# Kernel optimization log

Hardware: AMD Instinct MI355X
Metric: run time of the kernel (lower is better)

The kernel has to match this reference:

```python
import jax, jax.numpy as jnp
import numpy as np

B, N, D = 2, 2048, 1024
H, DH = 16, 64
EPS = 1e-5


def _layernorm(t, g, b):
    m = jnp.mean(t, axis=-1, keepdims=True)
    v = jnp.mean(jnp.square(t - m), axis=-1, keepdims=True)
    return (t - m) * jax.lax.rsqrt(v + EPS) * g + b


def setup_inputs() -> dict:
    key = jax.random.key(0)
    ks = jax.random.split(key, 4)
    return {
        "x": jax.random.normal(ks[0], (B, N, D), dtype=jnp.float32),
        "ln_g": jnp.ones((D,), jnp.float32),
        "ln_b": jnp.zeros((D,), jnp.float32),
        "lnc_g": jnp.ones((D,), jnp.float32),
        "lnc_b": jnp.zeros((D,), jnp.float32),
        "Wq": jax.random.normal(ks[1], (D, H * DH), jnp.float32) * 0.02,
        "Wkv": jax.random.normal(ks[2], (D, 2 * H * DH), jnp.float32) * 0.02,
        "Wo": jax.random.normal(ks[3], (H * DH, D), jnp.float32) * 0.02,
    }


def reference(x, ln_g, ln_b, lnc_g, lnc_b, Wq, Wkv, Wo):
    scale = DH ** (-0.5)
    xn = _layernorm(x, ln_g, ln_b)          # self-attn: context = x
    cn = _layernorm(x, lnc_g, lnc_b)
    q = xn @ Wq                              # [b, n, h*d]
    kv = cn @ Wkv
    k, v = jnp.split(kv, 2, axis=-1)
    # b n (h d) -> b h n d
    q = q.reshape(B, N, H, DH).transpose(0, 2, 1, 3)
    k = k.reshape(B, N, H, DH).transpose(0, 2, 1, 3)
    v = v.reshape(B, N, H, DH).transpose(0, 2, 1, 3)
    sim = jnp.einsum("bhnd,bhmd->bhnm", q, k) * scale
    neg = -jnp.finfo(sim.dtype).max
    causal = jnp.tril(jnp.ones((N, N), dtype=bool))  # allow j <= i
    sim = jnp.where(causal[None, None], sim, neg)
    attn = jax.nn.softmax(sim.astype(jnp.float32), axis=-1)
    out = jnp.einsum("bhnm,bhmd->bhnd", attn, v)
    out = out.transpose(0, 2, 1, 3).reshape(B, N, H * DH)
    return out @ Wo
```

## Files before the change

kernel.cpp:

```cpp
#include <hip/hip_runtime.h>
#include <hip/hip_bf16.h>

#define B_  2
#define N_  2048
#define D_  1024
#define H_  16
#define DH_ 64
#define BN_ROWS (B_ * N_)
#define EPS_ 1e-5f
#define QKV_N 3072

typedef __attribute__((ext_vector_type(8))) short bf16x8_t;
typedef __attribute__((ext_vector_type(4))) short bf16x4_t;
typedef __attribute__((ext_vector_type(4))) float f32x4_t;

#define MFMA16(a, b, c) __builtin_amdgcn_mfma_f32_16x16x16bf16_1k(a, b, c, 0, 0, 0)

typedef const unsigned int __attribute__((address_space(1)))* gas_ptr;
typedef unsigned int __attribute__((address_space(3)))* las_ptr;

__device__ __forceinline__ void async16(const unsigned short* g, unsigned short* l) {
    __builtin_amdgcn_global_load_lds((gas_ptr)g, (las_ptr)l, 16, 0, 0);
}

__device__ __forceinline__ unsigned short f2bf(float f) {
    unsigned int u = __float_as_uint(f);
    unsigned int r = u + 0x7FFFu + ((u >> 16) & 1u);
    return (unsigned short)(r >> 16);
}

__device__ __forceinline__ unsigned int pk2bf(float a, float b) {
    __hip_bfloat162 t = __float22bfloat162_rn(float2{a, b});
    return *(unsigned int*)&t;
}

__global__ __launch_bounds__(256) void ln_wt_kernel(
    const float* __restrict__ x,
    const float* __restrict__ g1, const float* __restrict__ b1,
    const float* __restrict__ g2, const float* __restrict__ b2,
    const float* __restrict__ Wq, const float* __restrict__ Wkv,
    const float* __restrict__ Wo,
    unsigned short* __restrict__ xn, unsigned short* __restrict__ cn,
    unsigned short* __restrict__ wqkvT, unsigned short* __restrict__ woT) {
    const int bid = blockIdx.x;
    const int tid = threadIdx.x;

    if (bid < BN_ROWS) {
        const int row = bid;
        const float4 v = ((const float4*)(x + (size_t)row * D_))[tid];

        float s  = v.x + v.y + v.z + v.w;
        float s2 = v.x * v.x + v.y * v.y + v.z * v.z + v.w * v.w;
        #pragma unroll
        for (int off = 32; off > 0; off >>= 1) {
            s  += __shfl_down(s,  off);
            s2 += __shfl_down(s2, off);
        }
        __shared__ float red[8];
        if ((tid & 63) == 0) { red[tid >> 6] = s; red[4 + (tid >> 6)] = s2; }
        __syncthreads();
        const float S  = red[0] + red[1] + red[2] + red[3];
        const float S2 = red[4] + red[5] + red[6] + red[7];
        const float mean = S * (1.0f / D_);
        const float var  = S2 * (1.0f / D_) - mean * mean;
        const float rstd = rsqrtf(var + EPS_);

        const float4 G1 = ((const float4*)g1)[tid];
        const float4 B1 = ((const float4*)b1)[tid];
        const float4 G2 = ((const float4*)g2)[tid];
        const float4 B2 = ((const float4*)b2)[tid];

        float nx[4] = { (v.x - mean) * rstd, (v.y - mean) * rstd,
                        (v.z - mean) * rstd, (v.w - mean) * rstd };
        ushort4 o1, o2;
        o1.x = f2bf(nx[0] * G1.x + B1.x); o1.y = f2bf(nx[1] * G1.y + B1.y);
        o1.z = f2bf(nx[2] * G1.z + B1.z); o1.w = f2bf(nx[3] * G1.w + B1.w);
        o2.x = f2bf(nx[0] * G2.x + B2.x); o2.y = f2bf(nx[1] * G2.y + B2.y);
        o2.z = f2bf(nx[2] * G2.z + B2.z); o2.w = f2bf(nx[3] * G2.w + B2.w);
        ((ushort4*)(xn + (size_t)row * D_))[tid] = o1;
        ((ushort4*)(cn + (size_t)row * D_))[tid] = o2;
    } else {
        const int zz = bid - BN_ROWS;
        const float* src;
        unsigned short* dst;
        int N, t;
        if (zz < 1024)      { src = Wq;  dst = wqkvT;                       N = 1024; t = zz; }
        else if (zz < 3072) { src = Wkv; dst = wqkvT + (size_t)1024 * 1024; N = 2048; t = zz - 1024; }
        else                { src = Wo;  dst = woT;                         N = 1024; t = zz - 3072; }
        const int nb = N / 32;
        const int n0 = (t % nb) * 32, k0 = (t / nb) * 32;

        __shared__ float tile[32][33];
        const int tx = tid & 31, ty = tid >> 5;
        #pragma unroll
        for (int i = 0; i < 4; i++)
            tile[ty + i * 8][tx] = src[(size_t)(k0 + ty + i * 8) * N + n0 + tx];
        __syncthreads();
        #pragma unroll
        for (int i = 0; i < 4; i++)
            dst[(size_t)(n0 + ty + i * 8) * 1024 + k0 + tx] = f2bf(tile[tx][ty + i * 8]);
    }
}

template <int BM, bool FUSED, bool BF16OUT, int MINW>
__global__ __launch_bounds__(256, MINW) void gemm_kernel(
    const unsigned short* __restrict__ A0, const unsigned short* __restrict__ A1,
    const unsigned short* __restrict__ Bt, void* __restrict__ Cv,
    unsigned short* __restrict__ vt, int M, int N, int K) {
    constexpr int WM = BM / 2, MT = WM / 16, AI = BM / 32;
    __shared__ unsigned short As[BM * 64];
    __shared__ unsigned short Bs[128 * 64];
    const int tid = threadIdx.x, lane = tid & 63, w = tid >> 6;
    const int quad = lane >> 4, l16 = lane & 15;
    const int lr8 = lane >> 3, pg8 = lane & 7;
    const int wr = (w >> 1) * WM, wc = (w & 1) * 64;
    const int bm = blockIdx.y * BM, bn = blockIdx.x * 128;
    const unsigned short* A = (FUSED && bn >= 1024) ? A1 : A0;
    const float cscale = (FUSED && bn < 1024) ? 0.180336880111120f : 1.0f;

    f32x4_t acc[MT][4] = {};
    for (int k0 = 0; k0 < K; k0 += 64) {
        #pragma unroll
        for (int i = 0; i < AI; i++) {
            const int rb = w * (BM / 4) + i * 8;
            const int r  = rb + lr8;
            const int g  = pg8 ^ (r & 7);
            async16(&A[(size_t)(bm + r) * K + k0 + g * 8], &As[rb * 64]);
        }
        #pragma unroll
        for (int i = 0; i < 4; i++) {
            const int rb = w * 32 + i * 8;
            const int r  = rb + lr8;
            const int g  = pg8 ^ (r & 7);
            async16(&Bt[(size_t)(bn + r) * K + k0 + g * 8], &Bs[rb * 64]);
        }
        __syncthreads();
        #pragma unroll
        for (int kk = 0; kk < 64; kk += 32) {
            bf16x8_t af[MT], bfr[4];
            const int g0 = (kk >> 3) + quad;
            #pragma unroll
            for (int t = 0; t < MT; t++)
                af[t] = *(const bf16x8_t*)&As[(wr + t * 16 + l16) * 64 +
                                              ((g0 ^ (l16 & 7)) * 8)];
            #pragma unroll
            for (int t = 0; t < 4; t++)
                bfr[t] = *(const bf16x8_t*)&Bs[(wc + t * 16 + l16) * 64 +
                                               ((g0 ^ (l16 & 7)) * 8)];
            #pragma unroll
            for (int mt = 0; mt < MT; mt++)
                #pragma unroll
                for (int nt = 0; nt < 4; nt++)
                    acc[mt][nt] = __builtin_amdgcn_mfma_f32_16x16x32_bf16(
                        af[mt], bfr[nt], acc[mt][nt], 0, 0, 0);
        }
        __syncthreads();
    }

    if (FUSED && bn >= 2048) {
        const int seq0 = bm + wr;
        const int bq = seq0 >> 11;
        const int kt = (seq0 & (N_ - 1)) >> 6;
        #pragma unroll
        for (int nt = 0; nt < 4; nt++) {
            const int c = (bn - 2048) + wc + nt * 16 + l16;
            unsigned short* dst =
                vt + (((size_t)(bq * 32 + kt) * 1024) + c) * 64;
            #pragma unroll
            for (int mt = 0; mt < 4; mt++) {
                uint2 v2 = { pk2bf(acc[mt][nt][0], acc[mt][nt][1]),
                             pk2bf(acc[mt][nt][2], acc[mt][nt][3]) };
                *(uint2*)&dst[mt * 16 + quad * 4] = v2;
            }
        }
        return;
    }

    #pragma unroll
    for (int mt = 0; mt < MT; mt++)
        #pragma unroll
        for (int nt = 0; nt < 4; nt++)
            #pragma unroll
            for (int r = 0; r < 4; r++) {
                const int row = bm + wr + mt * 16 + quad * 4 + r;
                const int col = bn + wc + nt * 16 + l16;
                if (BF16OUT)
                    ((unsigned short*)Cv)[(size_t)row * N + col] =
                        f2bf(acc[mt][nt][r] * cscale);
                else
                    ((float*)Cv)[(size_t)row * N + col] = acc[mt][nt][r];
            }
}

__global__ __launch_bounds__(256, 2) void flash_attn_kernel(
    const unsigned short* __restrict__ qkv, const unsigned short* __restrict__ vt,
    unsigned short* __restrict__ out) {
    __shared__ unsigned short Qs[64 * 64];
    __shared__ unsigned short Ks[2][64 * 64];
    __shared__ unsigned short Vts[3][64 * 64];

    const int tid = threadIdx.x, lane = tid & 63, w = tid >> 6;
    const int quad = lane >> 4, l16 = lane & 15;
    const int lr8 = lane >> 3, pg8 = lane & 7;
    const int bid = blockIdx.x;
    const int bh   = (bid & 7) * 4 + ((bid >> 3) & 3);
    const int pair = bid >> 5;
    const int b = bh >> 4, h = bh & 15;

    const unsigned short* qb  = qkv + (size_t)(b * N_) * QKV_N + h * DH_;
    const unsigned short* kb  = qb + 1024;
    const unsigned short* vtb = vt + ((size_t)(b * 32) * 1024 + h * 64) * 64;

    bf16x4_t ones4;
    #pragma unroll
    for (int j = 0; j < 4; j++) ones4[j] = (short)0x3F80;

    for (int phase = 0; phase < 2; phase++) {
        const int qt = phase ? (31 - pair) : pair;
        const int qs = qt * 64;
        const int niter = qt + 1;

        __syncthreads();

        f32x4_t o[4] = {};
        f32x4_t lacc = {};
        bf16x8_t qf[2];
        bf16x4_t pf[4];

        auto prefetch = [&](int t) {
            const int ksel = t & 1, vsel = t % 3;
            #pragma unroll
            for (int i = 0; i < 2; i++) {
                const int rb = w * 16 + i * 8;
                const int r  = rb + lr8;
                const int g  = pg8 ^ (r & 7);
                async16(&kb[(size_t)(t * 64 + r) * QKV_N + g * 8],
                        &Ks[ksel][rb * 64]);
                async16(&vtb[((size_t)t * 1024 + r) * 64 + g * 8],
                        &Vts[vsel][rb * 64]);
            }
        };
        auto do_qk = [&](int kbuf, f32x4_t* s) {
            __builtin_amdgcn_s_setprio(1);
            #pragma unroll
            for (int k2 = 0; k2 < 2; k2++) {
                const int g0 = k2 * 4 + quad;
                #pragma unroll
                for (int kt = 0; kt < 4; kt++) {
                    const bf16x8_t a = *(const bf16x8_t*)&Ks[kbuf][
                        (kt * 16 + l16) * 64 + (g0 ^ (l16 & 7)) * 8];
                    s[kt] = __builtin_amdgcn_mfma_f32_16x16x32_bf16(
                        a, qf[k2], s[kt], 0, 0, 0);
                }
            }
            __builtin_amdgcn_s_setprio(0);
        };
        auto do_exp = [&](const f32x4_t* s, int js, bool edge) {
            #pragma unroll
            for (int kt = 0; kt < 4; kt++) {
                float p[4];
                #pragma unroll
                for (int r = 0; r < 4; r++) {
                    float sv = s[kt][r];
                    if (edge) {
                        const int key = js + kt * 16 + quad * 4 + r;
                        const int qy  = qs + w * 16 + l16;
                        if (key > qy) sv = -3e38f;
                    }
                    p[r] = __builtin_amdgcn_exp2f(sv);
                }
                uint2 pk = { pk2bf(p[0], p[1]), pk2bf(p[2], p[3]) };
                pf[kt] = *(bf16x4_t*)&pk;
            }
        };
        auto do_pv = [&](int vbuf) {
            __builtin_amdgcn_s_setprio(1);
            #pragma unroll
            for (int kt = 0; kt < 4; kt++) {
                const int g = kt * 2 + (quad >> 1);
                const int col = ((g ^ (l16 & 7)) * 8) + (quad & 1) * 4;
                #pragma unroll
                for (int nt = 0; nt < 4; nt++) {
                    const bf16x4_t bv = *(const bf16x4_t*)&Vts[vbuf][
                        (nt * 16 + l16) * 64 + col];
                    o[nt] = MFMA16(pf[kt], bv, o[nt]);
                }
                lacc = MFMA16(pf[kt], ones4, lacc);
            }
            __builtin_amdgcn_s_setprio(0);
        };

        #pragma unroll
        for (int i = 0; i < 2; i++) {
            const int rb = w * 16 + i * 8;
            const int r  = rb + lr8;
            const int g  = pg8 ^ (r & 7);
            async16(&qb[(size_t)(qs + r) * QKV_N + g * 8], &Qs[rb * 64]);
        }
        prefetch(0);
        __syncthreads();

        if (niter > 1) prefetch(1);
        #pragma unroll
        for (int k2 = 0; k2 < 2; k2++) {
            const int g0 = k2 * 4 + quad;
            qf[k2] = *(const bf16x8_t*)&Qs[
                (w * 16 + l16) * 64 + (g0 ^ (l16 & 7)) * 8];
        }
        {
            f32x4_t s[4] = {};
            do_qk(0, s);
            do_exp(s, 0, niter == 1);
        }

        for (int jt = 1; jt < niter; jt++) {
            __syncthreads();
            if (jt + 1 < niter) prefetch(jt + 1);
            f32x4_t s[4] = {};
            do_qk(jt & 1, s);
            do_pv((jt - 1) % 3);
            do_exp(s, jt * 64, jt == niter - 1);
        }
        do_pv((niter - 1) % 3);

        #pragma unroll
        for (int r = 0; r < 4; r++) {
            const float inv = 1.0f / lacc[r];
            const int query = qs + w * 16 + quad * 4 + r;
            const int row = b * N_ + query;
            #pragma unroll
            for (int nt = 0; nt < 4; nt++) {
                const int col = h * DH_ + nt * 16 + l16;
                out[(size_t)row * (H_ * DH_) + col] = f2bf(o[nt][r] * inv);
            }
        }
    }
}

extern "C" void kernel_launch(void* const* d_in, const int* in_sizes, int n_in,
                              void* d_out, int out_size, void* d_ws, size_t ws_size,
                              hipStream_t stream) {
    const float* x     = (const float*)d_in[0];
    const float* ln_g  = (const float*)d_in[1];
    const float* ln_b  = (const float*)d_in[2];
    const float* lnc_g = (const float*)d_in[3];
    const float* lnc_b = (const float*)d_in[4];
    const float* Wq    = (const float*)d_in[5];
    const float* Wkv   = (const float*)d_in[6];
    const float* Wo    = (const float*)d_in[7];

    char* ws = (char*)d_ws;
    const size_t MB = 1024 * 1024;
    unsigned short* qkv   = (unsigned short*)(ws + 0 * MB);
    unsigned short* vtbuf = (unsigned short*)(ws + 24 * MB);
    unsigned short* xn    = (unsigned short*)(ws + 32 * MB);
    unsigned short* cn    = (unsigned short*)(ws + 40 * MB);
    unsigned short* wqkvT = (unsigned short*)(ws + 48 * MB);
    unsigned short* woT   = (unsigned short*)(ws + 54 * MB);
    unsigned short* ao    = xn;

    ln_wt_kernel<<<8192, 256, 0, stream>>>(
        x, ln_g, ln_b, lnc_g, lnc_b, Wq, Wkv, Wo, xn, cn, wqkvT, woT);

    gemm_kernel<128, true, true, 3>
        <<<dim3(QKV_N / 128, BN_ROWS / 128), 256, 0, stream>>>(
        xn, cn, wqkvT, qkv, vtbuf, BN_ROWS, QKV_N, D_);

    flash_attn_kernel<<<B_ * H_ * 16, 256, 0, stream>>>(qkv, vtbuf, ao);

    gemm_kernel<64, false, false, 2>
        <<<dim3(D_ / 128, BN_ROWS / 64), 256, 0, stream>>>(
        ao, nullptr, woT, (float*)d_out, nullptr, BN_ROWS, D_, H_ * DH_);
}
```

Measured before the change: 182.5 us.

## Split attention key tile across two wave groups with LDS reduction

Doubles the flash-attention block to 512 threads (8 waves), where each group of four waves handles half of each 64-key tile for the same 16 query rows. At the end, the partial output and row sums from the second group are written to shared memory and added by the first group before normalization and store. The goal is more waves per CU to hide latency and halve per-wave MFMA work per tile, at the cost of an extra LDS reduction, two extra barriers, and the removal of s_setprio hints. No max-subtraction is used, so the partial sums can be added directly.

```diff
diff --git a/kernel.cpp b/kernel.cpp
--- a/kernel.cpp
+++ b/kernel.cpp
@@ -192,7 +192,7 @@
             }
 }
 
-__global__ __launch_bounds__(256, 2) void flash_attn_kernel(
+__global__ __launch_bounds__(512, 4) void flash_attn_kernel(
     const unsigned short* __restrict__ qkv, const unsigned short* __restrict__ vt,
     unsigned short* __restrict__ out) {
     __shared__ unsigned short Qs[64 * 64];
@@ -202,6 +202,8 @@
     const int tid = threadIdx.x, lane = tid & 63, w = tid >> 6;
     const int quad = lane >> 4, l16 = lane & 15;
     const int lr8 = lane >> 3, pg8 = lane & 7;
+    const int wq = w & 3;
+    const int wk = w >> 2;
     const int bid = blockIdx.x;
     const int bh   = (bid & 7) * 4 + ((bid >> 3) & 3);
     const int pair = bid >> 5;
@@ -225,46 +227,41 @@
         f32x4_t o[4] = {};
         f32x4_t lacc = {};
         bf16x8_t qf[2];
-        bf16x4_t pf[4];
+        bf16x4_t pf[2];
 
         auto prefetch = [&](int t) {
             const int ksel = t & 1, vsel = t % 3;
-            #pragma unroll
-            for (int i = 0; i < 2; i++) {
-                const int rb = w * 16 + i * 8;
-                const int r  = rb + lr8;
-                const int g  = pg8 ^ (r & 7);
-                async16(&kb[(size_t)(t * 64 + r) * QKV_N + g * 8],
-                        &Ks[ksel][rb * 64]);
-                async16(&vtb[((size_t)t * 1024 + r) * 64 + g * 8],
-                        &Vts[vsel][rb * 64]);
-            }
+            const int rb = w * 8;
+            const int r  = rb + lr8;
+            const int g  = pg8 ^ (r & 7);
+            async16(&kb[(size_t)(t * 64 + r) * QKV_N + g * 8], &Ks[ksel][rb * 64]);
+            async16(&vtb[((size_t)t * 1024 + r) * 64 + g * 8], &Vts[vsel][rb * 64]);
         };
         auto do_qk = [&](int kbuf, f32x4_t* s) {
-            __builtin_amdgcn_s_setprio(1);
             #pragma unroll
             for (int k2 = 0; k2 < 2; k2++) {
                 const int g0 = k2 * 4 + quad;
                 #pragma unroll
-                for (int kt = 0; kt < 4; kt++) {
+                for (int kt = 0; kt < 2; kt++) {
+                    const int ktg = wk * 2 + kt;
                     const bf16x8_t a = *(const bf16x8_t*)&Ks[kbuf][
-                        (kt * 16 + l16) * 64 + (g0 ^ (l16 & 7)) * 8];
+                        (ktg * 16 + l16) * 64 + (g0 ^ (l16 & 7)) * 8];
                     s[kt] = __builtin_amdgcn_mfma_f32_16x16x32_bf16(
                         a, qf[k2], s[kt], 0, 0, 0);
                 }
             }
-            __builtin_amdgcn_s_setprio(0);
         };
         auto do_exp = [&](const f32x4_t* s, int js, bool edge) {
             #pragma unroll
-            for (int kt = 0; kt < 4; kt++) {
+            for (int kt = 0; kt < 2; kt++) {
+                const int ktg = wk * 2 + kt;
                 float p[4];
                 #pragma unroll
                 for (int r = 0; r < 4; r++) {
                     float sv = s[kt][r];
                     if (edge) {
-                        const int key = js + kt * 16 + quad * 4 + r;
-                        const int qy  = qs + w * 16 + l16;
+                        const int key = js + ktg * 16 + quad * 4 + r;
+                        const int qy  = qs + wq * 16 + l16;
                         if (key > qy) sv = -3e38f;
                     }
                     p[r] = __builtin_amdgcn_exp2f(sv);
@@ -274,10 +271,10 @@
             }
         };
         auto do_pv = [&](int vbuf) {
-            __builtin_amdgcn_s_setprio(1);
-            #pragma unroll
-            for (int kt = 0; kt < 4; kt++) {
-                const int g = kt * 2 + (quad >> 1);
+            #pragma unroll
+            for (int kt = 0; kt < 2; kt++) {
+                const int ktg = wk * 2 + kt;
+                const int g = ktg * 2 + (quad >> 1);
                 const int col = ((g ^ (l16 & 7)) * 8) + (quad & 1) * 4;
                 #pragma unroll
                 for (int nt = 0; nt < 4; nt++) {
@@ -287,12 +284,10 @@
                 }
                 lacc = MFMA16(pf[kt], ones4, lacc);
             }
-            __builtin_amdgcn_s_setprio(0);
         };
 
-        #pragma unroll
-        for (int i = 0; i < 2; i++) {
-            const int rb = w * 16 + i * 8;
+        {
+            const int rb = w * 8;
             const int r  = rb + lr8;
             const int g  = pg8 ^ (r & 7);
             async16(&qb[(size_t)(qs + r) * QKV_N + g * 8], &Qs[rb * 64]);
@@ -305,10 +300,10 @@
         for (int k2 = 0; k2 < 2; k2++) {
             const int g0 = k2 * 4 + quad;
             qf[k2] = *(const bf16x8_t*)&Qs[
-                (w * 16 + l16) * 64 + (g0 ^ (l16 & 7)) * 8];
+                (wq * 16 + l16) * 64 + (g0 ^ (l16 & 7)) * 8];
         }
         {
-            f32x4_t s[4] = {};
+            f32x4_t s[2] = {};
             do_qk(0, s);
             do_exp(s, 0, niter == 1);
         }
@@ -316,22 +311,43 @@
         for (int jt = 1; jt < niter; jt++) {
             __syncthreads();
             if (jt + 1 < niter) prefetch(jt + 1);
-            f32x4_t s[4] = {};
+            f32x4_t s[2] = {};
             do_qk(jt & 1, s);
             do_pv((jt - 1) % 3);
             do_exp(s, jt * 64, jt == niter - 1);
         }
         do_pv((niter - 1) % 3);
 
-        #pragma unroll
-        for (int r = 0; r < 4; r++) {
-            const float inv = 1.0f / lacc[r];
-            const int query = qs + w * 16 + quad * 4 + r;
-            const int row = b * N_ + query;
-            #pragma unroll
-            for (int nt = 0; nt < 4; nt++) {
-                const int col = h * DH_ + nt * 16 + l16;
-                out[(size_t)row * (H_ * DH_) + col] = f2bf(o[nt][r] * inv);
+        __syncthreads();
+        float* red = (float*)&Vts[0][0];
+        if (wk == 1) {
+            #pragma unroll
+            for (int r = 0; r < 4; r++) {
+                const int q = quad * 4 + r;
+                const int base = (wq * 16 + q) * 68;
+                #pragma unroll
+                for (int nt = 0; nt < 4; nt++)
+                    red[base + nt * 16 + l16] = o[nt][r];
+                red[base + 64] = lacc[r];
+            }
+        }
+        __syncthreads();
+        if (wk == 0) {
+            #pragma unroll
+            for (int r = 0; r < 4; r++) {
+                const int q = quad * 4 + r;
+                const int base = (wq * 16 + q) * 68;
+                #pragma unroll
+                for (int nt = 0; nt < 4; nt++)
+                    o[nt][r] += red[base + nt * 16 + l16];
+                const float inv = 1.0f / (lacc[r] + red[base + 64]);
+                const int query = qs + wq * 16 + quad * 4 + r;
+                const int row = b * N_ + query;
+                #pragma unroll
+                for (int nt = 0; nt < 4; nt++) {
+                    const int col = h * DH_ + nt * 16 + l16;
+                    out[(size_t)row * (H_ * DH_) + col] = f2bf(o[nt][r] * inv);
+                }
             }
         }
     }
@@ -366,7 +382,7 @@
         <<<dim3(QKV_N / 128, BN_ROWS / 128), 256, 0, stream>>>(
         xn, cn, wqkvT, qkv, vtbuf, BN_ROWS, QKV_N, D_);
 
-    flash_attn_kernel<<<B_ * H_ * 16, 256, 0, stream>>>(qkv, vtbuf, ao);
+    flash_attn_kernel<<<B_ * H_ * 16, 512, 0, stream>>>(qkv, vtbuf, ao);
 
     gemm_kernel<64, false, false, 2>
         <<<dim3(D_ / 128, BN_ROWS / 64), 256, 0, stream>>>(
```

Result: faster. 175.7 us (-3.7%).
